# Performance work log

Measured on AMD Instinct MI355X. Metric: run time of the kernel, lower is better.

Reference implementation:

```python
import jax, jax.numpy as jnp
import numpy as np

B, S, D, H = 2, 2048, 1024, 16
HD = D // H

def setup_inputs() -> dict:
    key = jax.random.key(0)
    ks = jax.random.split(key, 6)
    s = 1.0 / np.sqrt(D)
    return {
        "inputs": jax.random.normal(ks[0], (B, S, D), dtype=jnp.float32),
        "Wq": jax.random.normal(ks[1], (D, D), dtype=jnp.float32) * s,
        "Wk": jax.random.normal(ks[2], (D, D), dtype=jnp.float32) * s,
        "Wv": jax.random.normal(ks[3], (D, D), dtype=jnp.float32) * s,
        "Wo": jax.random.normal(ks[4], (D, D), dtype=jnp.float32) * s,
        "bo": jax.random.normal(ks[5], (D,), dtype=jnp.float32) * 0.01,
    }

def reference(inputs, Wq, Wk, Wv, Wo, bo):
    b, n, _ = inputs.shape
    # Linear projections (torch Linear: x @ W.T), reshape to [b, H, n, hd]
    def proj(W):
        return (inputs @ W.T).reshape(b, n, H, HD).transpose(0, 2, 1, 3)
    q, k, v = proj(Wq), proj(Wk), proj(Wv)
    scores = jnp.einsum('bhqd,bhkd->bhqk', q, k)  # [b,H,n,n]
    causal = jnp.triu(jnp.ones((n, n), dtype=bool), k=1)
    scores = jnp.where(causal, -jnp.inf, scores)
    w = jax.nn.softmax(scores / np.sqrt(HD), axis=-1)
    ctx = jnp.einsum('bhqk,bhkd->bhqd', w, v)
    ctx = ctx.transpose(0, 2, 1, 3).reshape(b, n, D)
    return ctx @ Wo.T + bo
```

## Files before the change

kernel.cpp:

```cpp
#include <hip/hip_runtime.h>
#include <hip/hip_bf16.h>
#include <stdint.h>

#define B_   2
#define S_   2048
#define D_   1024
#define H_   16
#define LOG2E 1.4426950408889634f

using f32x4  = __attribute__((ext_vector_type(4))) float;
using short8 = __attribute__((ext_vector_type(8))) short;

__device__ __forceinline__ unsigned short f2bf(float x) {
    unsigned u = __builtin_bit_cast(unsigned, x);
    u += 0x7fffu + ((u >> 16) & 1u);
    return (unsigned short)(u >> 16);
}

__device__ __forceinline__ unsigned cvt_pk_bf16(float lo, float hi) {
    unsigned r;
    asm("v_cvt_pk_bf16_f32 %0, %1, %2" : "=v"(r) : "v"(lo), "v"(hi));
    return r;
}

__device__ __forceinline__ float fast_exp2(float x) {
    float r;
    asm("v_exp_f32 %0, %1" : "=v"(r) : "v"(x));
    return r;
}

__device__ __forceinline__ float fast_rcp(float x) {
    float r;
    asm("v_rcp_f32 %0, %1" : "=v"(r) : "v"(x));
    return r;
}

__device__ __forceinline__ void gll16(const void* g, void* l) {
    __builtin_amdgcn_global_load_lds(
        (const __attribute__((address_space(1))) void*)(uintptr_t)g,
        (__attribute__((address_space(3))) void*)(uint32_t)(uintptr_t)l,
        16, 0, 0);
}

#define MFMA_BF16(a, b, c) __builtin_amdgcn_mfma_f32_16x16x32_bf16((a), (b), (c), 0, 0, 0)

__global__ __launch_bounds__(256)
void conv_all_kernel(const float* __restrict__ X,
                     const float* __restrict__ Wq, const float* __restrict__ Wk,
                     const float* __restrict__ Wv, const float* __restrict__ Wo,
                     short* __restrict__ Xb, short* __restrict__ Wqkv,
                     short* __restrict__ Wob) {
    const int bid = blockIdx.x;
    const float* src;
    short* dst;
    float sc = 1.0f;
    int i;
    if (bid < 2048) {
        src = X; dst = Xb; i = bid * 256 + threadIdx.x;
    } else {
        int wv = bid - 2048;
        int which = wv >> 9;
        src = (which == 0) ? Wq : (which == 1) ? Wk : (which == 2) ? Wv : Wo;
        dst = (which == 3) ? Wob : (Wqkv + (size_t)which * D_ * D_);
        if (which == 0) sc = 0.125f * LOG2E;
        i = (wv & 511) * 256 + threadIdx.x;
    }
    const float4* s4 = (const float4*)src;
    float4 a = s4[i * 2];
    float4 b = s4[i * 2 + 1];
    union { unsigned short u[8]; short8 v; } o;
    o.u[0] = f2bf(a.x * sc); o.u[1] = f2bf(a.y * sc); o.u[2] = f2bf(a.z * sc); o.u[3] = f2bf(a.w * sc);
    o.u[4] = f2bf(b.x * sc); o.u[5] = f2bf(b.y * sc); o.u[6] = f2bf(b.z * sc); o.u[7] = f2bf(b.w * sc);
    ((short8*)dst)[i] = o.v;
}

__global__ __launch_bounds__(512, 4)
void gemm_qkv128_kernel(const short* __restrict__ X, const short* __restrict__ Wqkv,
                        short* __restrict__ Qo, short* __restrict__ Ko,
                        short* __restrict__ VTo)
{
    __shared__ short sA[2][128 * 64];
    __shared__ short sB[2][128 * 64];
    const int cid = blockIdx.x;
    const int swz = (cid & 7) * 96 + (cid >> 3);
    const int n0 = (swz % 24) * 128;
    const int m0 = (swz / 24) * 128;
    const int tid = threadIdx.x, lane = tid & 63, w = tid >> 6;
    const int wm = w >> 2, wn = w & 3;
    const int l15 = lane & 15, lg = lane >> 4;

#define STAGE_Q(buf, kt) do {                                                  \
        int k0_ = (kt) << 6;                                                   \
        _Pragma("unroll")                                                      \
        for (int it_ = 0; it_ < 2; ++it_) {                                    \
            int g_ = it_ * 512 + tid;                                          \
            int r_ = g_ >> 3, s_ = g_ & 7;                                     \
            int sb_ = s_ ^ (r_ & 7);                                           \
            int dst_ = (it_ * 512 + w * 64) * 16;                              \
            gll16(X    + (size_t)(m0 + r_) * D_ + k0_ + sb_ * 8,               \
                  (char*)sA[buf] + dst_);                                      \
            gll16(Wqkv + (size_t)(n0 + r_) * D_ + k0_ + sb_ * 8,               \
                  (char*)sB[buf] + dst_);                                      \
        }                                                                      \
    } while (0)

    const f32x4 z4 = {0.f, 0.f, 0.f, 0.f};
    f32x4 acc[4][2];
    #pragma unroll
    for (int i = 0; i < 4; ++i)
        #pragma unroll
        for (int j = 0; j < 2; ++j) acc[i][j] = z4;

    STAGE_Q(0, 0);
    STAGE_Q(1, 1);

    for (int t = 0; t < 16; ++t) {
        if (t < 15) { asm volatile("s_waitcnt vmcnt(4)" ::: "memory"); }
        else        { asm volatile("s_waitcnt vmcnt(0)" ::: "memory"); }
        __builtin_amdgcn_sched_barrier(0);
        __builtin_amdgcn_s_barrier();
        __builtin_amdgcn_sched_barrier(0);
        const short* a  = sA[t & 1];
        const short* bm = sB[t & 1];
        #pragma unroll
        for (int ks = 0; ks < 2; ++ks) {
            short8 af[4], bf[2];
            #pragma unroll
            for (int i = 0; i < 4; ++i) {
                int r = wm * 64 + i * 16 + l15;
                af[i] = *(const short8*)(a + r * 64 + ((((ks << 2) + lg) ^ (r & 7)) << 3));
            }
            #pragma unroll
            for (int j = 0; j < 2; ++j) {
                int r = wn * 32 + j * 16 + l15;
                bf[j] = *(const short8*)(bm + r * 64 + ((((ks << 2) + lg) ^ (r & 7)) << 3));
            }
            __builtin_amdgcn_s_setprio(1);
            #pragma unroll
            for (int i = 0; i < 4; ++i)
                #pragma unroll
                for (int j = 0; j < 2; ++j)
                    acc[i][j] = MFMA_BF16(af[i], bf[j], acc[i][j]);
            __builtin_amdgcn_s_setprio(0);
        }
        asm volatile("s_waitcnt lgkmcnt(0)" ::: "memory");
        __builtin_amdgcn_sched_barrier(0);
        __builtin_amdgcn_s_barrier();
        __builtin_amdgcn_sched_barrier(0);
        if (t + 2 < 16) STAGE_Q(t & 1, t + 2);
    }
#undef STAGE_Q

    const int z = n0 >> 10;
    if (z < 2) {
        short* Out = (z == 0) ? Qo : Ko;
        #pragma unroll
        for (int j = 0; j < 2; ++j) {
            int n = n0 + wn * 32 + j * 16 + l15;
            int h = (n >> 6) & 15, hd = n & 63;
            #pragma unroll
            for (int i = 0; i < 4; ++i)
                #pragma unroll
                for (int r = 0; r < 4; ++r) {
                    int m = m0 + wm * 64 + i * 16 + lg * 4 + r;
                    int b = m >> 11, s = m & (S_ - 1);
                    Out[(((size_t)b * H_ + h) * S_ + s) * 64 + hd] = (short)f2bf(acc[i][j][r]);
                }
        }
    } else {
        #pragma unroll
        for (int j = 0; j < 2; ++j) {
            int n = n0 + wn * 32 + j * 16 + l15;
            int h = (n >> 6) & 15, hd = n & 63;
            #pragma unroll
            for (int i = 0; i < 4; ++i) {
                int m = m0 + wm * 64 + i * 16 + lg * 4;
                int b = m >> 11, s0 = m & (S_ - 1);
                union { unsigned u32[2]; unsigned long long q64; } pk;
                pk.u32[0] = cvt_pk_bf16(acc[i][j][0], acc[i][j][1]);
                pk.u32[1] = cvt_pk_bf16(acc[i][j][2], acc[i][j][3]);
                *(unsigned long long*)(VTo + (((size_t)b * H_ + h) * 64 + hd) * S_ + s0) = pk.q64;
            }
        }
    }
}

__global__ __launch_bounds__(512, 4)
void gemm_out_kernel(const short* __restrict__ CTX, const short* __restrict__ Wob,
                     const float* __restrict__ bias, float* __restrict__ out)
{
    __shared__ short sA[2][128 * 64];
    __shared__ short sB[2][128 * 64];
    const int cid = blockIdx.y * 8 + blockIdx.x;
    const int swz = (cid & 7) * 32 + (cid >> 3);
    const int n0 = (swz & 7) * 128;
    const int m0 = (swz >> 3) * 128;
    const int tid = threadIdx.x, lane = tid & 63, w = tid >> 6;
    const int wm = w >> 2, wn = w & 3;
    const int l15 = lane & 15, lg = lane >> 4;

#define STAGE_O(buf, kt) do {                                                  \
        int k0_ = (kt) << 6;                                                   \
        _Pragma("unroll")                                                      \
        for (int it_ = 0; it_ < 2; ++it_) {                                    \
            int g_ = it_ * 512 + tid;                                          \
            int r_ = g_ >> 3, s_ = g_ & 7;                                     \
            int sb_ = s_ ^ (r_ & 7);                                           \
            int dst_ = (it_ * 512 + w * 64) * 16;                              \
            gll16(CTX + (size_t)(m0 + r_) * D_ + k0_ + sb_ * 8,                \
                  (char*)sA[buf] + dst_);                                      \
            gll16(Wob + (size_t)(n0 + r_) * D_ + k0_ + sb_ * 8,                \
                  (char*)sB[buf] + dst_);                                      \
        }                                                                      \
    } while (0)

    const f32x4 z4 = {0.f, 0.f, 0.f, 0.f};
    f32x4 acc[4][2];
    #pragma unroll
    for (int i = 0; i < 4; ++i)
        #pragma unroll
        for (int j = 0; j < 2; ++j) acc[i][j] = z4;

    STAGE_O(0, 0);
    STAGE_O(1, 1);

    for (int t = 0; t < 16; ++t) {
        if (t < 15) { asm volatile("s_waitcnt vmcnt(4)" ::: "memory"); }
        else        { asm volatile("s_waitcnt vmcnt(0)" ::: "memory"); }
        __builtin_amdgcn_sched_barrier(0);
        __builtin_amdgcn_s_barrier();
        __builtin_amdgcn_sched_barrier(0);
        const short* a  = sA[t & 1];
        const short* bm = sB[t & 1];
        #pragma unroll
        for (int ks = 0; ks < 2; ++ks) {
            short8 af[4], bf[2];
            #pragma unroll
            for (int i = 0; i < 4; ++i) {
                int r = wm * 64 + i * 16 + l15;
                af[i] = *(const short8*)(a + r * 64 + ((((ks << 2) + lg) ^ (r & 7)) << 3));
            }
            #pragma unroll
            for (int j = 0; j < 2; ++j) {
                int r = wn * 32 + j * 16 + l15;
                bf[j] = *(const short8*)(bm + r * 64 + ((((ks << 2) + lg) ^ (r & 7)) << 3));
            }
            __builtin_amdgcn_s_setprio(1);
            #pragma unroll
            for (int i = 0; i < 4; ++i)
                #pragma unroll
                for (int j = 0; j < 2; ++j)
                    acc[i][j] = MFMA_BF16(af[i], bf[j], acc[i][j]);
            __builtin_amdgcn_s_setprio(0);
        }
        asm volatile("s_waitcnt lgkmcnt(0)" ::: "memory");
        __builtin_amdgcn_sched_barrier(0);
        __builtin_amdgcn_s_barrier();
        __builtin_amdgcn_sched_barrier(0);
        if (t + 2 < 16) STAGE_O(t & 1, t + 2);
    }
#undef STAGE_O

    #pragma unroll
    for (int j = 0; j < 2; ++j) {
        int n = n0 + wn * 32 + j * 16 + l15;
        float bn = bias[n];
        #pragma unroll
        for (int i = 0; i < 4; ++i)
            #pragma unroll
            for (int r = 0; r < 4; ++r) {
                int m = m0 + wm * 64 + i * 16 + lg * 4 + r;
                out[(size_t)m * D_ + n] = acc[i][j][r] + bn;
            }
    }
}

__global__ __launch_bounds__(256, 4)
void attn_kernel(const short* __restrict__ Q, const short* __restrict__ K,
                 const short* __restrict__ VT, short* __restrict__ CTX)
{
    __shared__ short Kb[2][4096];
    __shared__ short Vb[2][4096];
    __shared__ char  Pl[4 * 2048];
    const int idx = blockIdx.x;
    const int k4  = idx >> 8;
    const int u   = idx & 255;
    const int v   = u >> 5;
    const int bh  = u & 31;
    const int ht  = (k4 == 0) ? v : (k4 == 1) ? (15 - v)
                  : (k4 == 2) ? (16 + v) : (31 - v);
    const int b  = bh >> 4, h = bh & 15;
    const int tid = threadIdx.x, lane = tid & 63, w = tid >> 6;
    const int l15 = lane & 15, lg = lane >> 4;
    const short* Qg = Q  + (size_t)bh * S_ * 64;
    const short* Kg = K  + (size_t)bh * S_ * 64;
    const short* Vg = VT + (size_t)bh * 64 * S_;
    char* Pw = Pl + w * 2048;

    const int qb = ht * 64 + w * 16;
    const int nt = ht + 1;

#define STAGE_KV(bufidx, ktile) do {                                         \
        int kt64_ = (ktile) << 6;                                            \
        _Pragma("unroll")                                                    \
        for (int it_ = 0; it_ < 2; ++it_) {                                  \
            int g_ = it_ * 256 + tid;                                        \
            int row_ = g_ >> 3, jb_ = g_ & 7;                                \
            int sj_ = jb_ ^ (row_ & 7);                                      \
            int base_ = (it_ * 256 + w * 64) * 16;                           \
            gll16(Kg + (size_t)(kt64_ + row_) * 64 + sj_ * 8,                \
                  (char*)Kb[bufidx] + base_);                                \
            gll16(Vg + (size_t)row_ * S_ + kt64_ + sj_ * 8,                  \
                  (char*)Vb[bufidx] + base_);                                \
        }                                                                    \
    } while (0)

    short8 qf[2];
    #pragma unroll
    for (int ks = 0; ks < 2; ++ks)
        qf[ks] = *(const short8*)(Qg + (size_t)(qb + l15) * 64 + ks * 32 + lg * 8);

    const short8 ones8 = { (short)0x3F80, (short)0x3F80, (short)0x3F80, (short)0x3F80,
                           (short)0x3F80, (short)0x3F80, (short)0x3F80, (short)0x3F80 };
    const f32x4 z4 = {0.f, 0.f, 0.f, 0.f};
    f32x4 o[4];
    f32x4 o5 = z4;
    #pragma unroll
    for (int nf = 0; nf < 4; ++nf) o[nf] = z4;

    STAGE_KV(0, 0);
    STAGE_KV(1, 1);

    for (int t = 0; t < nt; ++t) {
        if (t + 1 < nt) { asm volatile("s_waitcnt vmcnt(4)" ::: "memory"); }
        else            { asm volatile("s_waitcnt vmcnt(0)" ::: "memory"); }
        __builtin_amdgcn_sched_barrier(0);
        __builtin_amdgcn_s_barrier();
        __builtin_amdgcn_sched_barrier(0);
        const short* kb = Kb[t & 1];
        const short* vb = Vb[t & 1];
        const int kt = t << 6;

        {
            f32x4 sv[4] = {z4, z4, z4, z4};
            __builtin_amdgcn_s_setprio(1);
            #pragma unroll
            for (int ks = 0; ks < 2; ++ks)
                #pragma unroll
                for (int nf = 0; nf < 4; ++nf) {
                    int rr = nf * 16 + l15;
                    short8 kf = *(const short8*)((const char*)kb + rr * 128 +
                                                 (((ks << 2) + lg) ^ (rr & 7)) * 16);
                    sv[nf] = MFMA_BF16(kf, qf[ks], sv[nf]);
                }
            __builtin_amdgcn_s_setprio(0);
            if (kt + 63 > qb) {
                int q = qb + l15;
                #pragma unroll
                for (int nf = 0; nf < 4; ++nf)
                    #pragma unroll
                    for (int r = 0; r < 4; ++r)
                        if (kt + nf * 16 + lg * 4 + r > q) sv[nf][r] = -3e38f;
            }
            #pragma unroll
            for (int nf = 0; nf < 4; ++nf)
                #pragma unroll
                for (int r = 0; r < 4; ++r)
                    sv[nf][r] = fast_exp2(sv[nf][r]);
            #pragma unroll
            for (int nf = 0; nf < 4; ++nf) {
                union { unsigned u32[2]; unsigned long long q64; } pk;
                pk.u32[0] = cvt_pk_bf16(sv[nf][0], sv[nf][1]);
                pk.u32[1] = cvt_pk_bf16(sv[nf][2], sv[nf][3]);
                int kby = (nf * 16 + lg * 4) * 2;
                int off = l15 * 128 + (((kby >> 4) ^ (l15 & 7)) << 4) + (kby & 15);
                *(unsigned long long*)(Pw + off) = pk.q64;
            }
            #pragma unroll
            for (int ks = 0; ks < 2; ++ks) {
                int off = l15 * 128 + ((((ks << 2) + lg) ^ (l15 & 7)) << 4);
                short8 af = *(const short8*)(Pw + off);
                __builtin_amdgcn_s_setprio(1);
                #pragma unroll
                for (int nf = 0; nf < 4; ++nf) {
                    int rr = nf * 16 + l15;
                    short8 vf = *(const short8*)((const char*)vb + rr * 128 +
                                                 (((ks << 2) + lg) ^ (rr & 7)) * 16);
                    o[nf] = MFMA_BF16(af, vf, o[nf]);
                }
                o5 = MFMA_BF16(af, ones8, o5);
                __builtin_amdgcn_s_setprio(0);
            }
        }
        asm volatile("s_waitcnt lgkmcnt(0)" ::: "memory");
        __builtin_amdgcn_sched_barrier(0);
        __builtin_amdgcn_s_barrier();
        __builtin_amdgcn_sched_barrier(0);
        if (t + 2 < nt) STAGE_KV(t & 1, t + 2);
    }
#undef STAGE_KV

    #pragma unroll
    for (int r = 0; r < 4; ++r) {
        float inv = fast_rcp(o5[r]);
        int s = qb + lg * 4 + r;
        size_t base = ((size_t)b * S_ + s) * D_ + h * 64;
        #pragma unroll
        for (int nf = 0; nf < 4; ++nf)
            CTX[base + nf * 16 + l15] = (short)f2bf(o[nf][r] * inv);
    }
}

extern "C" void kernel_launch(void* const* d_in, const int* in_sizes, int n_in,
                              void* d_out, int out_size, void* d_ws, size_t ws_size,
                              hipStream_t stream) {
    const float* X  = (const float*)d_in[0];
    const float* Wq = (const float*)d_in[1];
    const float* Wk = (const float*)d_in[2];
    const float* Wv = (const float*)d_in[3];
    const float* Wo = (const float*)d_in[4];
    const float* bo = (const float*)d_in[5];
    float* out = (float*)d_out;

    char* ws = (char*)d_ws;
    const size_t MB = 1024 * 1024;
    short* Xb   = (short*)(ws);
    short* CTXw = (short*)(ws);
    short* Wqkv = (short*)(ws +  8 * MB);
    short* Wob  = (short*)(ws + 14 * MB);
    short* Qw   = (short*)(ws + 16 * MB);
    short* Kw   = (short*)(ws + 24 * MB);
    short* VTw  = (short*)(ws + 32 * MB);

    conv_all_kernel<<<4096, 256, 0, stream>>>(X, Wq, Wk, Wv, Wo, Xb, Wqkv, Wob);

    gemm_qkv128_kernel<<<768, 512, 0, stream>>>(Xb, Wqkv, Qw, Kw, VTw);

    attn_kernel<<<1024, 256, 0, stream>>>(Qw, Kw, VTw, CTXw);

    gemm_out_kernel<<<dim3(8, 32), 512, 0, stream>>>(CTXw, Wob, bo, out);
}
```

Before: 86.99 us.

## Replace double-buffered 512-thread QKV GEMM with single-buffer 256-thread 64x64 warp tiles

Rewrites the QKV projection GEMM to use 256 threads per block, with each wave computing a 64x64 sub-tile (4x4 MFMAs) instead of 64x32. Shared memory drops to a single buffer and the manual async prefetch pipeline with vmcnt waits is removed in favour of load, syncthreads, compute, syncthreads. The larger per-wave tile gives more MFMA work per LDS fragment load and halves the LDS footprint. In exchange, global loads no longer overlap with compute inside a block, so latency hiding depends on other resident blocks, and the extra accumulators raise register pressure.

```diff
diff --git a/kernel.cpp b/kernel.cpp
--- a/kernel.cpp
+++ b/kernel.cpp
@@ -74,89 +74,70 @@
     ((short8*)dst)[i] = o.v;
 }
 
-__global__ __launch_bounds__(512, 4)
-void gemm_qkv128_kernel(const short* __restrict__ X, const short* __restrict__ Wqkv,
-                        short* __restrict__ Qo, short* __restrict__ Ko,
-                        short* __restrict__ VTo)
+__global__ __launch_bounds__(256, 3)
+void gemm_qkv_m97_kernel(const short* __restrict__ X, const short* __restrict__ Wqkv,
+                         short* __restrict__ Qo, short* __restrict__ Ko,
+                         short* __restrict__ VTo)
 {
-    __shared__ short sA[2][128 * 64];
-    __shared__ short sB[2][128 * 64];
+    __shared__ short sA[128 * 64];
+    __shared__ short sB[128 * 64];
     const int cid = blockIdx.x;
     const int swz = (cid & 7) * 96 + (cid >> 3);
     const int n0 = (swz % 24) * 128;
     const int m0 = (swz / 24) * 128;
     const int tid = threadIdx.x, lane = tid & 63, w = tid >> 6;
-    const int wm = w >> 2, wn = w & 3;
+    const int wm = w & 1, wn = w >> 1;
     const int l15 = lane & 15, lg = lane >> 4;
 
-#define STAGE_Q(buf, kt) do {                                                  \
-        int k0_ = (kt) << 6;                                                   \
-        _Pragma("unroll")                                                      \
-        for (int it_ = 0; it_ < 2; ++it_) {                                    \
-            int g_ = it_ * 512 + tid;                                          \
-            int r_ = g_ >> 3, s_ = g_ & 7;                                     \
-            int sb_ = s_ ^ (r_ & 7);                                           \
-            int dst_ = (it_ * 512 + w * 64) * 16;                              \
-            gll16(X    + (size_t)(m0 + r_) * D_ + k0_ + sb_ * 8,               \
-                  (char*)sA[buf] + dst_);                                      \
-            gll16(Wqkv + (size_t)(n0 + r_) * D_ + k0_ + sb_ * 8,               \
-                  (char*)sB[buf] + dst_);                                      \
-        }                                                                      \
-    } while (0)
-
     const f32x4 z4 = {0.f, 0.f, 0.f, 0.f};
-    f32x4 acc[4][2];
+    f32x4 acc[4][4];
     #pragma unroll
     for (int i = 0; i < 4; ++i)
         #pragma unroll
-        for (int j = 0; j < 2; ++j) acc[i][j] = z4;
-
-    STAGE_Q(0, 0);
-    STAGE_Q(1, 1);
-
-    for (int t = 0; t < 16; ++t) {
-        if (t < 15) { asm volatile("s_waitcnt vmcnt(4)" ::: "memory"); }
-        else        { asm volatile("s_waitcnt vmcnt(0)" ::: "memory"); }
-        __builtin_amdgcn_sched_barrier(0);
-        __builtin_amdgcn_s_barrier();
-        __builtin_amdgcn_sched_barrier(0);
-        const short* a  = sA[t & 1];
-        const short* bm = sB[t & 1];
+        for (int j = 0; j < 4; ++j) acc[i][j] = z4;
+
+    for (int kt = 0; kt < 16; ++kt) {
+        const int k0 = kt << 6;
+        #pragma unroll
+        for (int it = 0; it < 4; ++it) {
+            int g = it * 256 + tid;
+            int r = g >> 3, s = g & 7;
+            int sb = s ^ (r & 7);
+            int dst = (it * 256 + w * 64) * 16;
+            gll16(X    + (size_t)(m0 + r) * D_ + k0 + sb * 8, (char*)sA + dst);
+            gll16(Wqkv + (size_t)(n0 + r) * D_ + k0 + sb * 8, (char*)sB + dst);
+        }
+        __syncthreads();
         #pragma unroll
         for (int ks = 0; ks < 2; ++ks) {
-            short8 af[4], bf[2];
+            short8 af[4], bf[4];
             #pragma unroll
             for (int i = 0; i < 4; ++i) {
                 int r = wm * 64 + i * 16 + l15;
-                af[i] = *(const short8*)(a + r * 64 + ((((ks << 2) + lg) ^ (r & 7)) << 3));
-            }
-            #pragma unroll
-            for (int j = 0; j < 2; ++j) {
-                int r = wn * 32 + j * 16 + l15;
-                bf[j] = *(const short8*)(bm + r * 64 + ((((ks << 2) + lg) ^ (r & 7)) << 3));
+                af[i] = *(const short8*)(sA + r * 64 + ((((ks << 2) + lg) ^ (r & 7)) << 3));
+            }
+            #pragma unroll
+            for (int j = 0; j < 4; ++j) {
+                int r = wn * 64 + j * 16 + l15;
+                bf[j] = *(const short8*)(sB + r * 64 + ((((ks << 2) + lg) ^ (r & 7)) << 3));
             }
             __builtin_amdgcn_s_setprio(1);
             #pragma unroll
             for (int i = 0; i < 4; ++i)
                 #pragma unroll
-                for (int j = 0; j < 2; ++j)
+                for (int j = 0; j < 4; ++j)
                     acc[i][j] = MFMA_BF16(af[i], bf[j], acc[i][j]);
             __builtin_amdgcn_s_setprio(0);
         }
-        asm volatile("s_waitcnt lgkmcnt(0)" ::: "memory");
-        __builtin_amdgcn_sched_barrier(0);
-        __builtin_amdgcn_s_barrier();
-        __builtin_amdgcn_sched_barrier(0);
-        if (t + 2 < 16) STAGE_Q(t & 1, t + 2);
-    }
-#undef STAGE_Q
+        __syncthreads();
+    }
 
     const int z = n0 >> 10;
     if (z < 2) {
         short* Out = (z == 0) ? Qo : Ko;
         #pragma unroll
-        for (int j = 0; j < 2; ++j) {
-            int n = n0 + wn * 32 + j * 16 + l15;
+        for (int j = 0; j < 4; ++j) {
+            int n = n0 + wn * 64 + j * 16 + l15;
             int h = (n >> 6) & 15, hd = n & 63;
             #pragma unroll
             for (int i = 0; i < 4; ++i)
@@ -169,8 +150,8 @@
         }
     } else {
         #pragma unroll
-        for (int j = 0; j < 2; ++j) {
-            int n = n0 + wn * 32 + j * 16 + l15;
+        for (int j = 0; j < 4; ++j) {
+            int n = n0 + wn * 64 + j * 16 + l15;
             int h = (n >> 6) & 15, hd = n & 63;
             #pragma unroll
             for (int i = 0; i < 4; ++i) {
@@ -434,7 +415,7 @@
 
     conv_all_kernel<<<4096, 256, 0, stream>>>(X, Wq, Wk, Wv, Wo, Xb, Wqkv, Wob);
 
-    gemm_qkv128_kernel<<<768, 512, 0, stream>>>(Xb, Wqkv, Qw, Kw, VTw);
+    gemm_qkv_m97_kernel<<<768, 256, 0, stream>>>(Xb, Wqkv, Qw, Kw, VTw);
 
     attn_kernel<<<1024, 256, 0, stream>>>(Qw, Kw, VTw, CTXw);
 
```

Result: no change. 86.42 us (-0.7%).
